# Performance work log

Measured on AMD Instinct MI355X. Metric: run time of the kernel, lower is better.

## Reference

```python
import jax, jax.numpy as jnp
import numpy as np

N, E = 100000, 1600000
IN, HID, OUT, HEADS = 128, 128, 64, 4
HD = HID // HEADS  # per-head dim = 32


def setup_inputs() -> dict:
    key = jax.random.key(0)
    ks = jax.random.split(key, 16)
    p = lambda k, shape: (jax.random.normal(k, shape, jnp.float32) * 0.1)
    return {
        "x": jax.random.normal(ks[0], (N, IN), jnp.float32),
        "edge_index": jax.random.randint(ks[1], (2, E), 0, N, dtype=jnp.int32),
        # layer 0: GATConv(IN -> HD per head, HEADS heads)
        "W0": p(ks[2], (IN, HID)), "b0": jnp.zeros((HID,), jnp.float32),
        "as0": p(ks[3], (HEADS, HD)), "ad0": p(ks[4], (HEADS, HD)),
        # layer 1: GATConv(HID -> HD per head, HEADS heads)
        "W1": p(ks[5], (HID, HID)), "b1": jnp.zeros((HID,), jnp.float32),
        "as1": p(ks[6], (HEADS, HD)), "ad1": p(ks[7], (HEADS, HD)),
        # layer 2: GATConv(HID -> OUT, 1 head)
        "W2": p(ks[8], (HID, OUT)), "b2": jnp.zeros((OUT,), jnp.float32),
        "as2": p(ks[9], (1, OUT)), "ad2": p(ks[10], (1, OUT)),
    }


def _gat_conv(x, W, b, a_src, a_dst, src, dst, heads):
    """PyG GATConv forward (shared src/dst projection, self-loops pre-added)."""
    n = x.shape[0]
    h = (x @ W).reshape(n, heads, -1)                    # [N, H, C]
    al_s = jnp.sum(h * a_src, axis=-1)                   # [N, H]
    al_d = jnp.sum(h * a_dst, axis=-1)                   # [N, H]
    e = jax.nn.leaky_relu(al_s[src] + al_d[dst], 0.2)    # [Etot, H]
    # softmax over incoming edges of each destination node
    m = jax.ops.segment_max(e, dst, num_segments=n)
    p = jnp.exp(e - m[dst])
    s = jax.ops.segment_sum(p, dst, num_segments=n)
    alpha = p / (s[dst] + 1e-16)                         # PyG softmax eps
    out = jax.ops.segment_sum(h[src] * alpha[:, :, None], dst, num_segments=n)
    return out.reshape(n, -1) + b


def _l1norm(x):
    # F.normalize(x, p=1.0): dim=1, eps=1e-12
    return x / jnp.maximum(jnp.sum(jnp.abs(x), axis=1, keepdims=True), 1e-12)


def reference(x, edge_index, W0, b0, as0, ad0, W1, b1, as1, ad1, W2, b2, as2, ad2):
    n = x.shape[0]
    loop = jnp.arange(n, dtype=edge_index.dtype)
    src = jnp.concatenate([edge_index[0], loop])  # GATConv add_self_loops=True
    dst = jnp.concatenate([edge_index[1], loop])
    # layer 0 (dropout=identity in eval; layernorm output is dead code in source)
    h = _gat_conv(x, W0, b0, as0, ad0, src, dst, HEADS)
    h = _l1norm(jax.nn.leaky_relu(h, 0.01))
    # layer 1 (residual + layernorm results are overwritten in source -> dead)
    h = _gat_conv(h, W1, b1, as1, ad1, src, dst, HEADS)
    h = jax.nn.leaky_relu(h, 0.01)
    # layer 2 (single head)
    h = _gat_conv(h, W2, b2, as2, ad2, src, dst, 1)
    return jax.nn.relu(_l1norm(h))
```

## Files before the change

kernel.cpp:

```cpp
#include <hip/hip_runtime.h>
#include <hip/hip_bf16.h>

#define NN 100000
#define NE 1600000
#define NB 391
#define CHUNK 4096

typedef short bf8v __attribute__((ext_vector_type(8)));
typedef float f32x4 __attribute__((ext_vector_type(4)));

static __device__ __forceinline__ float lrelu(float x, float s) {
    return x > 0.f ? x : s * x;
}

static __device__ __forceinline__ unsigned short f2b(float f) {
    __hip_bfloat16 b = __float2bfloat16(f);
    return *reinterpret_cast<unsigned short*>(&b);
}

struct alignas(4) bh2 {
    __hip_bfloat16 x, y;
};


__global__ __launch_bounds__(256) void bucket_hist(const int* __restrict__ dsts,
                                                   int* __restrict__ bcnt) {
    __shared__ int hist[NB];
    for (int t = threadIdx.x; t < NB; t += 256) hist[t] = 0;
    __syncthreads();
    int stride = gridDim.x * 256;
    for (int e = blockIdx.x * 256 + threadIdx.x; e < NE; e += stride)
        atomicAdd(&hist[dsts[e] >> 8], 1);
    __syncthreads();
    for (int t = threadIdx.x; t < NB; t += 256) {
        int c = hist[t];
        if (c) atomicAdd(&bcnt[t], c);
    }
}

__global__ __launch_bounds__(512) void bucket_scan(const int* __restrict__ bcnt,
                                                   int* __restrict__ bbase,
                                                   int* __restrict__ bcursor) {
    __shared__ int sd[512];
    int t = threadIdx.x;
    int v = (t < NB) ? bcnt[t] : 0;
    sd[t] = v;
    __syncthreads();
    for (int off = 1; off < 512; off <<= 1) {
        int x = (t >= off) ? sd[t - off] : 0;
        __syncthreads();
        sd[t] += x;
        __syncthreads();
    }
    int excl = sd[t] - v;
    if (t < NB) {
        bbase[t] = excl;
        bcursor[t] = excl;
    }
    if (t == NB - 1) bbase[NB] = excl + v;
}

__global__ __launch_bounds__(256) void partition_kernel(const int* __restrict__ srcs,
                                                        const int* __restrict__ dsts,
                                                        int* bcursor,
                                                        int2* __restrict__ part) {
    __shared__ int hist[NB];
    __shared__ int lbase[NB];
    for (int t = threadIdx.x; t < NB; t += 256) hist[t] = 0;
    __syncthreads();
    int e0 = blockIdx.x * CHUNK;
#pragma unroll
    for (int k = 0; k < CHUNK / 256; k++) {
        int e = e0 + k * 256 + threadIdx.x;
        if (e < NE) atomicAdd(&hist[dsts[e] >> 8], 1);
    }
    __syncthreads();
    for (int t = threadIdx.x; t < NB; t += 256) {
        int c = hist[t];
        if (c) lbase[t] = atomicAdd(&bcursor[t], c);
        hist[t] = 0;
    }
    __syncthreads();
#pragma unroll
    for (int k = 0; k < CHUNK / 256; k++) {
        int e = e0 + k * 256 + threadIdx.x;
        if (e < NE) {
            int s = srcs[e], d = dsts[e];
            int b = d >> 8;
            int r = atomicAdd(&hist[b], 1);
            part[lbase[b] + r] = make_int2(s, d);
        }
    }
}

__global__ __launch_bounds__(256) void bucket_fill(const int2* __restrict__ part,
                                                   const int* __restrict__ bbase,
                                                   int* __restrict__ offs,
                                                   int* __restrict__ csr) {
    __shared__ int lcur[256];
    __shared__ int sd[256];
    int b = blockIdx.x;
    int t = threadIdx.x;
    int ebeg = bbase[b], eend = bbase[b + 1];
    int node0 = b << 8;
    int nNodes = min(256, NN - node0);
    lcur[t] = 0;
    __syncthreads();
    for (int e = ebeg + t; e < eend; e += 256) {
        int2 p = part[e];
        atomicAdd(&lcur[p.y - node0], 1);
    }
    __syncthreads();
    int cnt = lcur[t];
    sd[t] = cnt;
    __syncthreads();
    for (int off = 1; off < 256; off <<= 1) {
        int x = (t >= off) ? sd[t - off] : 0;
        __syncthreads();
        sd[t] += x;
        __syncthreads();
    }
    int start = ebeg + sd[t] - cnt;
    if (t < nNodes) offs[node0 + t] = start;
    if (b == NB - 1 && t == 0) offs[NN] = NE;
    lcur[t] = start;
    __syncthreads();
    for (int e = ebeg + t; e < eend; e += 256) {
        int2 p = part[e];
        int pos = atomicAdd(&lcur[p.y - node0], 1);
        csr[pos] = p.x;
    }
}


template <int NOUT, int HEADS, bool AF32>
__global__ __launch_bounds__(256) void gemm_fused(
    const float* __restrict__ A32, const unsigned short* __restrict__ A16,
    const float* __restrict__ W, const float* __restrict__ asrc,
    const float* __restrict__ adst, unsigned short* __restrict__ h16out,
    float* __restrict__ als, float* __restrict__ ald, int n) {
    constexpr int NF = NOUT / 16;
    constexpr int PITCH = 136;
    __shared__ unsigned short Wl[NOUT * PITCH];

    const int tid = threadIdx.x;
    for (int i = tid; i < (128 * NOUT) / 4; i += 256) {
        int idx = i * 4;
        int k = idx / NOUT;
        int c = idx - k * NOUT;
        float4 wv = *(const float4*)&W[idx];
        Wl[(c + 0) * PITCH + k] = f2b(wv.x);
        Wl[(c + 1) * PITCH + k] = f2b(wv.y);
        Wl[(c + 2) * PITCH + k] = f2b(wv.z);
        Wl[(c + 3) * PITCH + k] = f2b(wv.w);
    }
    __syncthreads();

    const int lane = tid & 63, wave = tid >> 6;
    const int c = lane & 15, hi = lane >> 4;
    const int r0 = blockIdx.x * 64;
    const int arow = min(r0 + wave * 16 + c, n - 1);
    const int kb = hi * 8;

    f32x4 acc[NF];
#pragma unroll
    for (int nf = 0; nf < NF; ++nf) acc[nf] = 0;

#pragma unroll
    for (int kc = 0; kc < 4; ++kc) {
        bf8v a;
        if constexpr (AF32) {
            const float* ap = A32 + (size_t)arow * 128 + kc * 32 + kb;
            float4 f0 = *(const float4*)ap;
            float4 f1 = *(const float4*)(ap + 4);
            union {
                bf8v v;
                unsigned short u[8];
            } ua;
            ua.u[0] = f2b(f0.x);
            ua.u[1] = f2b(f0.y);
            ua.u[2] = f2b(f0.z);
            ua.u[3] = f2b(f0.w);
            ua.u[4] = f2b(f1.x);
            ua.u[5] = f2b(f1.y);
            ua.u[6] = f2b(f1.z);
            ua.u[7] = f2b(f1.w);
            a = ua.v;
        } else {
            a = *(const bf8v*)(A16 + (size_t)arow * 128 + kc * 32 + kb);
        }
#pragma unroll
        for (int nf = 0; nf < NF; ++nf) {
            bf8v b = *(const bf8v*)&Wl[(nf * 16 + c) * PITCH + kc * 32 + kb];
            acc[nf] = __builtin_amdgcn_mfma_f32_16x16x32_bf16(a, b, acc[nf], 0, 0, 0);
        }
    }

    float aS[NF], aD[NF];
#pragma unroll
    for (int nf = 0; nf < NF; ++nf) {
        aS[nf] = asrc[nf * 16 + c];
        aD[nf] = adst[nf * 16 + c];
    }
    float sRes[HEADS][4], dRes[HEADS][4];
#pragma unroll
    for (int hh = 0; hh < HEADS; ++hh) {
#pragma unroll
        for (int reg = 0; reg < 4; ++reg) {
            float s = 0.f, d = 0.f;
#pragma unroll
            for (int nf = hh * (NF / HEADS); nf < (hh + 1) * (NF / HEADS); ++nf) {
                s += acc[nf][reg] * aS[nf];
                d += acc[nf][reg] * aD[nf];
            }
#pragma unroll
            for (int o = 1; o < 16; o <<= 1) {
                s += __shfl_xor(s, o);
                d += __shfl_xor(d, o);
            }
            sRes[hh][reg] = s;
            dRes[hh][reg] = d;
        }
    }
    if (c == 0) {
#pragma unroll
        for (int reg = 0; reg < 4; ++reg) {
            int ro = r0 + wave * 16 + hi * 4 + reg;
            if (ro < n) {
                if constexpr (HEADS == 4) {
                    *(float4*)&als[ro * 4] =
                        make_float4(sRes[0][reg], sRes[1][reg], sRes[2][reg], sRes[3][reg]);
                    *(float4*)&ald[ro * 4] =
                        make_float4(dRes[0][reg], dRes[1][reg], dRes[2][reg], dRes[3][reg]);
                } else {
                    als[ro] = sRes[0][reg];
                    ald[ro] = dRes[0][reg];
                }
            }
        }
    }

    __syncthreads();
#pragma unroll
    for (int nf = 0; nf < NF; ++nf) {
#pragma unroll
        for (int reg = 0; reg < 4; ++reg) {
            int rl = wave * 16 + hi * 4 + reg;
            Wl[rl * PITCH + nf * 16 + c] = f2b(acc[nf][reg]);
        }
    }
    __syncthreads();
    constexpr int SEGS = NOUT / 8;
    for (int i = tid; i < 64 * SEGS; i += 256) {
        int rl = i / SEGS, sg = i - rl * SEGS;
        int ro = r0 + rl;
        if (ro < n)
            *(uint4*)&h16out[(size_t)ro * NOUT + sg * 8] =
                *(const uint4*)&Wl[rl * PITCH + sg * 8];
    }
}


__global__ __launch_bounds__(256) void agg4_kernel(
    const char* __restrict__ hb, const float* __restrict__ als, const float* __restrict__ ald,
    const int* __restrict__ offs, const int* __restrict__ cur, const int* __restrict__ csr,
    const float* __restrict__ bias, __hip_bfloat16* __restrict__ out, int n, int do_l1) {
    __shared__ int soff[4][64];
    __shared__ float sp[4][64][4];
    int w = threadIdx.x >> 6;
    int v = blockIdx.x * 4 + w;
    if (v >= n) return;
    int lane = threadIdx.x & 63;
    int hd = lane >> 4;
    int lane4 = lane << 2;

    float4 av = *(const float4*)&ald[v * 4];
    float4 svv = *(const float4*)&als[v * 4];
    int begin = offs[v], end = cur[v];

    float ps0 = __expf(lrelu(svv.x + av.x, 0.2f));
    float ps1 = __expf(lrelu(svv.y + av.y, 0.2f));
    float ps2 = __expf(lrelu(svv.z + av.z, 0.2f));
    float ps3 = __expf(lrelu(svv.w + av.w, 0.2f));
    float psel = hd == 0 ? ps0 : hd == 1 ? ps1 : hd == 2 ? ps2 : ps3;
    unsigned uv = *(const unsigned*)(hb + (size_t)v * 256 + lane4);
    float acc0 = psel * __uint_as_float(uv << 16);
    float acc1 = psel * __uint_as_float(uv & 0xFFFF0000u);
    float s0 = 0.f, s1 = 0.f, s2 = 0.f, s3 = 0.f;

    for (int base = begin; base < end; base += 64) {
        int idx = base + lane;
        int cnt = min(64, end - base);
        if (idx < end) {
            int s = csr[idx];
            float4 q = *(const float4*)&als[s * 4];
            float p0 = __expf(lrelu(q.x + av.x, 0.2f));
            float p1 = __expf(lrelu(q.y + av.y, 0.2f));
            float p2 = __expf(lrelu(q.z + av.z, 0.2f));
            float p3 = __expf(lrelu(q.w + av.w, 0.2f));
            soff[w][lane] = s << 8;
            sp[w][lane][0] = p0;
            sp[w][lane][1] = p1;
            sp[w][lane][2] = p2;
            sp[w][lane][3] = p3;
            s0 += p0; s1 += p1; s2 += p2; s3 += p3;
        }
        asm volatile("s_waitcnt lgkmcnt(0)" ::: "memory");
        int t = 0;
        for (; t + 8 <= cnt; t += 8) {
            int o0 = soff[w][t + 0], o1 = soff[w][t + 1];
            int o2 = soff[w][t + 2], o3 = soff[w][t + 3];
            int o4 = soff[w][t + 4], o5 = soff[w][t + 5];
            int o6 = soff[w][t + 6], o7 = soff[w][t + 7];
            float p0 = sp[w][t + 0][hd], p1 = sp[w][t + 1][hd];
            float p2 = sp[w][t + 2][hd], p3 = sp[w][t + 3][hd];
            float p4 = sp[w][t + 4][hd], p5 = sp[w][t + 5][hd];
            float p6 = sp[w][t + 6][hd], p7 = sp[w][t + 7][hd];
            unsigned u0 = *(const unsigned*)(hb + o0 + lane4);
            unsigned u1 = *(const unsigned*)(hb + o1 + lane4);
            unsigned u2 = *(const unsigned*)(hb + o2 + lane4);
            unsigned u3 = *(const unsigned*)(hb + o3 + lane4);
            unsigned u4 = *(const unsigned*)(hb + o4 + lane4);
            unsigned u5 = *(const unsigned*)(hb + o5 + lane4);
            unsigned u6 = *(const unsigned*)(hb + o6 + lane4);
            unsigned u7 = *(const unsigned*)(hb + o7 + lane4);
            acc0 += p0 * __uint_as_float(u0 << 16);
            acc1 += p0 * __uint_as_float(u0 & 0xFFFF0000u);
            acc0 += p1 * __uint_as_float(u1 << 16);
            acc1 += p1 * __uint_as_float(u1 & 0xFFFF0000u);
            acc0 += p2 * __uint_as_float(u2 << 16);
            acc1 += p2 * __uint_as_float(u2 & 0xFFFF0000u);
            acc0 += p3 * __uint_as_float(u3 << 16);
            acc1 += p3 * __uint_as_float(u3 & 0xFFFF0000u);
            acc0 += p4 * __uint_as_float(u4 << 16);
            acc1 += p4 * __uint_as_float(u4 & 0xFFFF0000u);
            acc0 += p5 * __uint_as_float(u5 << 16);
            acc1 += p5 * __uint_as_float(u5 & 0xFFFF0000u);
            acc0 += p6 * __uint_as_float(u6 << 16);
            acc1 += p6 * __uint_as_float(u6 & 0xFFFF0000u);
            acc0 += p7 * __uint_as_float(u7 << 16);
            acc1 += p7 * __uint_as_float(u7 & 0xFFFF0000u);
        }
        for (; t < cnt; ++t) {
            int oa = soff[w][t];
            float pa = sp[w][t][hd];
            unsigned ua = *(const unsigned*)(hb + oa + lane4);
            acc0 += pa * __uint_as_float(ua << 16);
            acc1 += pa * __uint_as_float(ua & 0xFFFF0000u);
        }
    }
#pragma unroll
    for (int o = 32; o > 0; o >>= 1) {
        s0 += __shfl_xor(s0, o);
        s1 += __shfl_xor(s1, o);
        s2 += __shfl_xor(s2, o);
        s3 += __shfl_xor(s3, o);
    }
    s0 += ps0; s1 += ps1; s2 += ps2; s3 += ps3;
    float ssel = hd == 0 ? s0 : hd == 1 ? s1 : hd == 2 ? s2 : s3;
    float inv = 1.f / (ssel + 1e-16f);
    float2 bv = *(const float2*)&bias[2 * lane];
    float o0 = lrelu(acc0 * inv + bv.x, 0.01f);
    float o1 = lrelu(acc1 * inv + bv.y, 0.01f);
    if (do_l1) {
        float t = fabsf(o0) + fabsf(o1);
#pragma unroll
        for (int o = 32; o > 0; o >>= 1) t += __shfl_xor(t, o);
        float li = 1.f / fmaxf(t, 1e-12f);
        o0 *= li;
        o1 *= li;
    }
    bh2 pk;
    pk.x = __float2bfloat16(o0);
    pk.y = __float2bfloat16(o1);
    *(bh2*)&out[(size_t)v * 128 + 2 * lane] = pk;
}


__global__ __launch_bounds__(256) void agg1_kernel(
    const char* __restrict__ hb, const float* __restrict__ als, const float* __restrict__ ald,
    const int* __restrict__ offs, const int* __restrict__ cur, const int* __restrict__ csr,
    const float* __restrict__ bias, float* __restrict__ out, int n) {
    __shared__ int soff[4][64];
    __shared__ float sp[4][64];
    int w = threadIdx.x >> 6;
    int v = blockIdx.x * 4 + w;
    if (v >= n) return;
    int lane = threadIdx.x & 63;
    int lane2 = lane << 1;
    float aldv = ald[v];
    float alsv = als[v];
    int begin = offs[v], end = cur[v];

    float pself = __expf(lrelu(alsv + aldv, 0.2f));
    unsigned short usv = *(const unsigned short*)(hb + (size_t)v * 128 + lane2);
    float acc = pself * __uint_as_float(((unsigned)usv) << 16);
    float ssum = 0.f;

    for (int base = begin; base < end; base += 64) {
        int idx = base + lane;
        int cnt = min(64, end - base);
        if (idx < end) {
            int s = csr[idx];
            float p = __expf(lrelu(als[s] + aldv, 0.2f));
            soff[w][lane] = s << 7;
            sp[w][lane] = p;
            ssum += p;
        }
        asm volatile("s_waitcnt lgkmcnt(0)" ::: "memory");
        int t = 0;
        for (; t + 8 <= cnt; t += 8) {
            int o0 = soff[w][t + 0], o1 = soff[w][t + 1];
            int o2 = soff[w][t + 2], o3 = soff[w][t + 3];
            int o4 = soff[w][t + 4], o5 = soff[w][t + 5];
            int o6 = soff[w][t + 6], o7 = soff[w][t + 7];
            float p0 = sp[w][t + 0], p1 = sp[w][t + 1];
            float p2 = sp[w][t + 2], p3 = sp[w][t + 3];
            float p4 = sp[w][t + 4], p5 = sp[w][t + 5];
            float p6 = sp[w][t + 6], p7 = sp[w][t + 7];
            unsigned short u0 = *(const unsigned short*)(hb + o0 + lane2);
            unsigned short u1 = *(const unsigned short*)(hb + o1 + lane2);
            unsigned short u2 = *(const unsigned short*)(hb + o2 + lane2);
            unsigned short u3 = *(const unsigned short*)(hb + o3 + lane2);
            unsigned short u4 = *(const unsigned short*)(hb + o4 + lane2);
            unsigned short u5 = *(const unsigned short*)(hb + o5 + lane2);
            unsigned short u6 = *(const unsigned short*)(hb + o6 + lane2);
            unsigned short u7 = *(const unsigned short*)(hb + o7 + lane2);
            acc += p0 * __uint_as_float(((unsigned)u0) << 16);
            acc += p1 * __uint_as_float(((unsigned)u1) << 16);
            acc += p2 * __uint_as_float(((unsigned)u2) << 16);
            acc += p3 * __uint_as_float(((unsigned)u3) << 16);
            acc += p4 * __uint_as_float(((unsigned)u4) << 16);
            acc += p5 * __uint_as_float(((unsigned)u5) << 16);
            acc += p6 * __uint_as_float(((unsigned)u6) << 16);
            acc += p7 * __uint_as_float(((unsigned)u7) << 16);
        }
        for (; t < cnt; ++t) {
            int oa = soff[w][t];
            float pa = sp[w][t];
            unsigned short ua = *(const unsigned short*)(hb + oa + lane2);
            acc += pa * __uint_as_float(((unsigned)ua) << 16);
        }
    }
#pragma unroll
    for (int o = 32; o > 0; o >>= 1) ssum += __shfl_xor(ssum, o);
    ssum += pself;
    float o = acc / (ssum + 1e-16f) + bias[lane];
    float t = fabsf(o);
#pragma unroll
    for (int off = 32; off > 0; off >>= 1) t += __shfl_xor(t, off);
    o = o / fmaxf(t, 1e-12f);
    out[(size_t)v * 64 + lane] = fmaxf(o, 0.f);
}


extern "C" void kernel_launch(void* const* d_in, const int* in_sizes, int n_in,
                              void* d_out, int out_size, void* d_ws, size_t ws_size,
                              hipStream_t stream) {
    const float* x = (const float*)d_in[0];
    const int* ei = (const int*)d_in[1];
    const float* W0 = (const float*)d_in[2];
    const float* b0 = (const float*)d_in[3];
    const float* as0 = (const float*)d_in[4];
    const float* ad0 = (const float*)d_in[5];
    const float* W1 = (const float*)d_in[6];
    const float* b1 = (const float*)d_in[7];
    const float* as1 = (const float*)d_in[8];
    const float* ad1 = (const float*)d_in[9];
    const float* W2 = (const float*)d_in[10];
    const float* b2 = (const float*)d_in[11];
    const float* as2 = (const float*)d_in[12];
    const float* ad2 = (const float*)d_in[13];
    float* outp = (float*)d_out;

    char* ws = (char*)d_ws;
    size_t off = 0;
    auto alloc = [&](size_t bytes) -> void* {
        void* p = ws + off;
        off = (off + bytes + 255) & ~(size_t)255;
        return p;
    };
    int* offs = (int*)alloc((NN + 1) * 4);
    int* bcnt = (int*)alloc(NB * 4);
    int* bbase = (int*)alloc((NB + 1) * 4);
    int* bcursor = (int*)alloc(NB * 4);
    int2* part = (int2*)alloc((size_t)NE * 8);
    int* csr = (int*)alloc((size_t)NE * 4);
    unsigned short* h16 = (unsigned short*)alloc((size_t)NN * 128 * 2);
    unsigned short* a16 = (unsigned short*)alloc((size_t)NN * 128 * 2);
    float* als = (float*)alloc(NN * 4 * 4);
    float* ald = (float*)alloc(NN * 4 * 4);

    const int* srcs = ei;
    const int* dsts = ei + NE;

    hipMemsetAsync(bcnt, 0, NB * 4, stream);
    bucket_hist<<<NB, 256, 0, stream>>>(dsts, bcnt);
    bucket_scan<<<1, 512, 0, stream>>>(bcnt, bbase, bcursor);
    partition_kernel<<<(NE + CHUNK - 1) / CHUNK, 256, 0, stream>>>(srcs, dsts, bcursor, part);
    bucket_fill<<<NB, 256, 0, stream>>>(part, bbase, offs, csr);

    int ggrid = (NN + 63) / 64;
    int aggrid = (NN + 3) / 4;

    gemm_fused<128, 4, true><<<ggrid, 256, 0, stream>>>(x, nullptr, W0, as0, ad0, h16, als, ald,
                                                        NN);
    agg4_kernel<<<aggrid, 256, 0, stream>>>((const char*)h16, als, ald, offs, offs + 1, csr, b0,
                                            (__hip_bfloat16*)a16, NN, 1);
    gemm_fused<128, 4, false><<<ggrid, 256, 0, stream>>>(nullptr, a16, W1, as1, ad1, h16, als,
                                                         ald, NN);
    agg4_kernel<<<aggrid, 256, 0, stream>>>((const char*)h16, als, ald, offs, offs + 1, csr, b1,
                                            (__hip_bfloat16*)a16, NN, 0);
    gemm_fused<64, 1, false><<<ggrid, 256, 0, stream>>>(nullptr, a16, W2, as2, ad2, h16, als,
                                                        ald, NN);
    agg1_kernel<<<aggrid, 256, 0, stream>>>((const char*)h16, als, ald, offs, offs + 1, csr, b2,
                                            outp, NN);
}
```

Baseline: 381.8 us.

## Gather multiple edges per wavefront with wider 8-byte feature loads in aggregation

Both aggregation kernels now split each 64-lane wavefront into sub-groups. Each sub-group processes a different neighbor edge and loads 8 bytes (4 bf16) per lane instead of 2 or 4 bytes. Partial accumulators are combined with cross-lane shuffles at the end, and only the first sub-group writes the output with vectorized stores. The aim is fewer, wider gather instructions and fewer serialized loop iterations per edge chunk. The cost is extra shuffles, zero-padding of the shared-memory slots, and more accumulator registers.

```diff
diff --git a/kernel.cpp b/kernel.cpp
--- a/kernel.cpp
+++ b/kernel.cpp
@@ -18,9 +18,12 @@
     return *reinterpret_cast<unsigned short*>(&b);
 }
 
-struct alignas(4) bh2 {
-    __hip_bfloat16 x, y;
-};
+static __device__ __forceinline__ float blo(unsigned u) {
+    return __uint_as_float(u << 16);
+}
+static __device__ __forceinline__ float bhi(unsigned u) {
+    return __uint_as_float(u & 0xFFFF0000u);
+}
 
 
 __global__ __launch_bounds__(256) void bucket_hist(const int* __restrict__ dsts,
@@ -271,8 +274,10 @@
     int v = blockIdx.x * 4 + w;
     if (v >= n) return;
     int lane = threadIdx.x & 63;
-    int hd = lane >> 4;
-    int lane4 = lane << 2;
+    int half = lane >> 5;
+    int sl = lane & 31;
+    int hd = sl >> 3;
+    int fb = sl << 3;
 
     float4 av = *(const float4*)&ald[v * 4];
     float4 svv = *(const float4*)&als[v * 4];
@@ -283,9 +288,12 @@
     float ps2 = __expf(lrelu(svv.z + av.z, 0.2f));
     float ps3 = __expf(lrelu(svv.w + av.w, 0.2f));
     float psel = hd == 0 ? ps0 : hd == 1 ? ps1 : hd == 2 ? ps2 : ps3;
-    unsigned uv = *(const unsigned*)(hb + (size_t)v * 256 + lane4);
-    float acc0 = psel * __uint_as_float(uv << 16);
-    float acc1 = psel * __uint_as_float(uv & 0xFFFF0000u);
+    float pseed = (half == 0) ? psel : 0.f;
+    uint2 uv = *(const uint2*)(hb + (size_t)v * 256 + fb);
+    float acc0 = pseed * blo(uv.x);
+    float acc1 = pseed * bhi(uv.x);
+    float acc2 = pseed * blo(uv.y);
+    float acc3 = pseed * bhi(uv.y);
     float s0 = 0.f, s1 = 0.f, s2 = 0.f, s3 = 0.f;
 
     for (int base = begin; base < end; base += 64) {
@@ -304,51 +312,60 @@
             sp[w][lane][2] = p2;
             sp[w][lane][3] = p3;
             s0 += p0; s1 += p1; s2 += p2; s3 += p3;
+        } else {
+            soff[w][lane] = 0;
+            sp[w][lane][0] = 0.f;
+            sp[w][lane][1] = 0.f;
+            sp[w][lane][2] = 0.f;
+            sp[w][lane][3] = 0.f;
         }
         asm volatile("s_waitcnt lgkmcnt(0)" ::: "memory");
+        int npair = (cnt + 1) >> 1;
         int t = 0;
-        for (; t + 8 <= cnt; t += 8) {
-            int o0 = soff[w][t + 0], o1 = soff[w][t + 1];
-            int o2 = soff[w][t + 2], o3 = soff[w][t + 3];
-            int o4 = soff[w][t + 4], o5 = soff[w][t + 5];
-            int o6 = soff[w][t + 6], o7 = soff[w][t + 7];
-            float p0 = sp[w][t + 0][hd], p1 = sp[w][t + 1][hd];
-            float p2 = sp[w][t + 2][hd], p3 = sp[w][t + 3][hd];
-            float p4 = sp[w][t + 4][hd], p5 = sp[w][t + 5][hd];
-            float p6 = sp[w][t + 6][hd], p7 = sp[w][t + 7][hd];
-            unsigned u0 = *(const unsigned*)(hb + o0 + lane4);
-            unsigned u1 = *(const unsigned*)(hb + o1 + lane4);
-            unsigned u2 = *(const unsigned*)(hb + o2 + lane4);
-            unsigned u3 = *(const unsigned*)(hb + o3 + lane4);
-            unsigned u4 = *(const unsigned*)(hb + o4 + lane4);
-            unsigned u5 = *(const unsigned*)(hb + o5 + lane4);
-            unsigned u6 = *(const unsigned*)(hb + o6 + lane4);
-            unsigned u7 = *(const unsigned*)(hb + o7 + lane4);
-            acc0 += p0 * __uint_as_float(u0 << 16);
-            acc1 += p0 * __uint_as_float(u0 & 0xFFFF0000u);
-            acc0 += p1 * __uint_as_float(u1 << 16);
-            acc1 += p1 * __uint_as_float(u1 & 0xFFFF0000u);
-            acc0 += p2 * __uint_as_float(u2 << 16);
-            acc1 += p2 * __uint_as_float(u2 & 0xFFFF0000u);
-            acc0 += p3 * __uint_as_float(u3 << 16);
-            acc1 += p3 * __uint_as_float(u3 & 0xFFFF0000u);
-            acc0 += p4 * __uint_as_float(u4 << 16);
-            acc1 += p4 * __uint_as_float(u4 & 0xFFFF0000u);
-            acc0 += p5 * __uint_as_float(u5 << 16);
-            acc1 += p5 * __uint_as_float(u5 & 0xFFFF0000u);
-            acc0 += p6 * __uint_as_float(u6 << 16);
-            acc1 += p6 * __uint_as_float(u6 & 0xFFFF0000u);
-            acc0 += p7 * __uint_as_float(u7 << 16);
-            acc1 += p7 * __uint_as_float(u7 & 0xFFFF0000u);
-        }
-        for (; t < cnt; ++t) {
-            int oa = soff[w][t];
-            float pa = sp[w][t][hd];
-            unsigned ua = *(const unsigned*)(hb + oa + lane4);
-            acc0 += pa * __uint_as_float(ua << 16);
-            acc1 += pa * __uint_as_float(ua & 0xFFFF0000u);
-        }
-    }
+        for (; t + 4 <= npair; t += 4) {
+            int e0 = 2 * (t + 0) + half;
+            int e1 = 2 * (t + 1) + half;
+            int e2 = 2 * (t + 2) + half;
+            int e3 = 2 * (t + 3) + half;
+            int o0 = soff[w][e0], o1 = soff[w][e1], o2 = soff[w][e2], o3 = soff[w][e3];
+            float p0 = sp[w][e0][hd], p1 = sp[w][e1][hd];
+            float p2 = sp[w][e2][hd], p3 = sp[w][e3][hd];
+            uint2 u0 = *(const uint2*)(hb + o0 + fb);
+            uint2 u1 = *(const uint2*)(hb + o1 + fb);
+            uint2 u2 = *(const uint2*)(hb + o2 + fb);
+            uint2 u3 = *(const uint2*)(hb + o3 + fb);
+            acc0 += p0 * blo(u0.x);
+            acc1 += p0 * bhi(u0.x);
+            acc2 += p0 * blo(u0.y);
+            acc3 += p0 * bhi(u0.y);
+            acc0 += p1 * blo(u1.x);
+            acc1 += p1 * bhi(u1.x);
+            acc2 += p1 * blo(u1.y);
+            acc3 += p1 * bhi(u1.y);
+            acc0 += p2 * blo(u2.x);
+            acc1 += p2 * bhi(u2.x);
+            acc2 += p2 * blo(u2.y);
+            acc3 += p2 * bhi(u2.y);
+            acc0 += p3 * blo(u3.x);
+            acc1 += p3 * bhi(u3.x);
+            acc2 += p3 * blo(u3.y);
+            acc3 += p3 * bhi(u3.y);
+        }
+        for (; t < npair; ++t) {
+            int e = 2 * t + half;
+            int o = soff[w][e];
+            float p = sp[w][e][hd];
+            uint2 u = *(const uint2*)(hb + o + fb);
+            acc0 += p * blo(u.x);
+            acc1 += p * bhi(u.x);
+            acc2 += p * blo(u.y);
+            acc3 += p * bhi(u.y);
+        }
+    }
+    acc0 += __shfl_xor(acc0, 32);
+    acc1 += __shfl_xor(acc1, 32);
+    acc2 += __shfl_xor(acc2, 32);
+    acc3 += __shfl_xor(acc3, 32);
 #pragma unroll
     for (int o = 32; o > 0; o >>= 1) {
         s0 += __shfl_xor(s0, o);
@@ -359,21 +376,27 @@
     s0 += ps0; s1 += ps1; s2 += ps2; s3 += ps3;
     float ssel = hd == 0 ? s0 : hd == 1 ? s1 : hd == 2 ? s2 : s3;
     float inv = 1.f / (ssel + 1e-16f);
-    float2 bv = *(const float2*)&bias[2 * lane];
+    float4 bv = *(const float4*)&bias[sl << 2];
     float o0 = lrelu(acc0 * inv + bv.x, 0.01f);
     float o1 = lrelu(acc1 * inv + bv.y, 0.01f);
+    float o2 = lrelu(acc2 * inv + bv.z, 0.01f);
+    float o3 = lrelu(acc3 * inv + bv.w, 0.01f);
     if (do_l1) {
-        float t = fabsf(o0) + fabsf(o1);
-#pragma unroll
-        for (int o = 32; o > 0; o >>= 1) t += __shfl_xor(t, o);
-        float li = 1.f / fmaxf(t, 1e-12f);
+        float tsum = fabsf(o0) + fabsf(o1) + fabsf(o2) + fabsf(o3);
+#pragma unroll
+        for (int o = 16; o > 0; o >>= 1) tsum += __shfl_xor(tsum, o);
+        float li = 1.f / fmaxf(tsum, 1e-12f);
         o0 *= li;
         o1 *= li;
-    }
-    bh2 pk;
-    pk.x = __float2bfloat16(o0);
-    pk.y = __float2bfloat16(o1);
-    *(bh2*)&out[(size_t)v * 128 + 2 * lane] = pk;
+        o2 *= li;
+        o3 *= li;
+    }
+    if (half == 0) {
+        uint2 pk;
+        pk.x = ((unsigned)f2b(o0)) | (((unsigned)f2b(o1)) << 16);
+        pk.y = ((unsigned)f2b(o2)) | (((unsigned)f2b(o3)) << 16);
+        *(uint2*)((char*)out + (size_t)v * 256 + fb) = pk;
+    }
 }
 
 
@@ -387,14 +410,20 @@
     int v = blockIdx.x * 4 + w;
     if (v >= n) return;
     int lane = threadIdx.x & 63;
-    int lane2 = lane << 1;
+    int grp = lane >> 4;
+    int sl = lane & 15;
+    int fb = sl << 3;
     float aldv = ald[v];
     float alsv = als[v];
     int begin = offs[v], end = cur[v];
 
     float pself = __expf(lrelu(alsv + aldv, 0.2f));
-    unsigned short usv = *(const unsigned short*)(hb + (size_t)v * 128 + lane2);
-    float acc = pself * __uint_as_float(((unsigned)usv) << 16);
+    float pseed = (grp == 0) ? pself : 0.f;
+    uint2 uv = *(const uint2*)(hb + (size_t)v * 128 + fb);
+    float acc0 = pseed * blo(uv.x);
+    float acc1 = pseed * bhi(uv.x);
+    float acc2 = pseed * blo(uv.y);
+    float acc3 = pseed * bhi(uv.y);
     float ssum = 0.f;
 
     for (int base = begin; base < end; base += 64) {
@@ -406,51 +435,66 @@
             soff[w][lane] = s << 7;
             sp[w][lane] = p;
             ssum += p;
+        } else {
+            soff[w][lane] = 0;
+            sp[w][lane] = 0.f;
         }
         asm volatile("s_waitcnt lgkmcnt(0)" ::: "memory");
+        int nq = (cnt + 3) >> 2;
         int t = 0;
-        for (; t + 8 <= cnt; t += 8) {
-            int o0 = soff[w][t + 0], o1 = soff[w][t + 1];
-            int o2 = soff[w][t + 2], o3 = soff[w][t + 3];
-            int o4 = soff[w][t + 4], o5 = soff[w][t + 5];
-            int o6 = soff[w][t + 6], o7 = soff[w][t + 7];
-            float p0 = sp[w][t + 0], p1 = sp[w][t + 1];
-            float p2 = sp[w][t + 2], p3 = sp[w][t + 3];
-            float p4 = sp[w][t + 4], p5 = sp[w][t + 5];
-            float p6 = sp[w][t + 6], p7 = sp[w][t + 7];
-            unsigned short u0 = *(const unsigned short*)(hb + o0 + lane2);
-            unsigned short u1 = *(const unsigned short*)(hb + o1 + lane2);
-            unsigned short u2 = *(const unsigned short*)(hb + o2 + lane2);
-            unsigned short u3 = *(const unsigned short*)(hb + o3 + lane2);
-            unsigned short u4 = *(const unsigned short*)(hb + o4 + lane2);
-            unsigned short u5 = *(const unsigned short*)(hb + o5 + lane2);
-            unsigned short u6 = *(const unsigned short*)(hb + o6 + lane2);
-            unsigned short u7 = *(const unsigned short*)(hb + o7 + lane2);
-            acc += p0 * __uint_as_float(((unsigned)u0) << 16);
-            acc += p1 * __uint_as_float(((unsigned)u1) << 16);
-            acc += p2 * __uint_as_float(((unsigned)u2) << 16);
-            acc += p3 * __uint_as_float(((unsigned)u3) << 16);
-            acc += p4 * __uint_as_float(((unsigned)u4) << 16);
-            acc += p5 * __uint_as_float(((unsigned)u5) << 16);
-            acc += p6 * __uint_as_float(((unsigned)u6) << 16);
-            acc += p7 * __uint_as_float(((unsigned)u7) << 16);
-        }
-        for (; t < cnt; ++t) {
-            int oa = soff[w][t];
-            float pa = sp[w][t];
-            unsigned short ua = *(const unsigned short*)(hb + oa + lane2);
-            acc += pa * __uint_as_float(((unsigned)ua) << 16);
-        }
-    }
+        for (; t + 2 <= nq; t += 2) {
+            int e0 = 4 * (t + 0) + grp;
+            int e1 = 4 * (t + 1) + grp;
+            int o0 = soff[w][e0], o1 = soff[w][e1];
+            float p0 = sp[w][e0], p1 = sp[w][e1];
+            uint2 u0 = *(const uint2*)(hb + o0 + fb);
+            uint2 u1 = *(const uint2*)(hb + o1 + fb);
+            acc0 += p0 * blo(u0.x);
+            acc1 += p0 * bhi(u0.x);
+            acc2 += p0 * blo(u0.y);
+            acc3 += p0 * bhi(u0.y);
+            acc0 += p1 * blo(u1.x);
+            acc1 += p1 * bhi(u1.x);
+            acc2 += p1 * blo(u1.y);
+            acc3 += p1 * bhi(u1.y);
+        }
+        for (; t < nq; ++t) {
+            int e = 4 * t + grp;
+            int o = soff[w][e];
+            float p = sp[w][e];
+            uint2 u = *(const uint2*)(hb + o + fb);
+            acc0 += p * blo(u.x);
+            acc1 += p * bhi(u.x);
+            acc2 += p * blo(u.y);
+            acc3 += p * bhi(u.y);
+        }
+    }
+    acc0 += __shfl_xor(acc0, 32);
+    acc1 += __shfl_xor(acc1, 32);
+    acc2 += __shfl_xor(acc2, 32);
+    acc3 += __shfl_xor(acc3, 32);
+    acc0 += __shfl_xor(acc0, 16);
+    acc1 += __shfl_xor(acc1, 16);
+    acc2 += __shfl_xor(acc2, 16);
+    acc3 += __shfl_xor(acc3, 16);
 #pragma unroll
     for (int o = 32; o > 0; o >>= 1) ssum += __shfl_xor(ssum, o);
     ssum += pself;
-    float o = acc / (ssum + 1e-16f) + bias[lane];
-    float t = fabsf(o);
-#pragma unroll
-    for (int off = 32; off > 0; off >>= 1) t += __shfl_xor(t, off);
-    o = o / fmaxf(t, 1e-12f);
-    out[(size_t)v * 64 + lane] = fmaxf(o, 0.f);
+    float inv = 1.f / (ssum + 1e-16f);
+    float4 bv = *(const float4*)&bias[sl << 2];
+    float o0 = acc0 * inv + bv.x;
+    float o1 = acc1 * inv + bv.y;
+    float o2 = acc2 * inv + bv.z;
+    float o3 = acc3 * inv + bv.w;
+    float tsum = fabsf(o0) + fabsf(o1) + fabsf(o2) + fabsf(o3);
+#pragma unroll
+    for (int o = 8; o > 0; o >>= 1) tsum += __shfl_xor(tsum, o);
+    float li = 1.f / fmaxf(tsum, 1e-12f);
+    if (grp == 0) {
+        *(float4*)&out[(size_t)v * 64 + (sl << 2)] =
+            make_float4(fmaxf(o0 * li, 0.f), fmaxf(o1 * li, 0.f), fmaxf(o2 * li, 0.f),
+                        fmaxf(o3 * li, 0.f));
+    }
 }
 
 
```

After: 416.2 us. +9.0%, slower.
